# Kernel optimization log

Hardware: AMD Instinct MI355X
Metric: run time of the kernel (lower is better)

The kernel has to match this reference:

```python
import jax, jax.numpy as jnp
import numpy as np

KS = {0: (6, 18), 1: (4, 12)}


def _build_modal_edges(feat, k_set):
    # feat: [N, C] -> H_modal [N, len(k_set)*N]
    N = feat.shape[0]
    f = feat / jnp.linalg.norm(feat, axis=1, keepdims=True).clip(1e-12)
    sim = f @ f.T  # [N, N] cosine similarity
    H_list = []
    cols_base = jnp.arange(N)
    for k in k_set:
        _, knn = jax.lax.top_k(sim, k + 1)  # [N, k+1]
        rows = knn.reshape(-1)
        cols = jnp.repeat(cols_base, k + 1)
        H = jnp.zeros((N, N), dtype=feat.dtype).at[rows, cols].set(1.0)
        H_list.append(H)
    return jnp.concatenate(H_list, axis=1)


def _build_incidence(feat1, feat2):
    # feat1/feat2: [N, C] (batch-mean features) -> H [2N, 5N]
    N = feat1.shape[0]
    H1 = _build_modal_edges(feat1, KS[0])  # [N, 2N]
    H2 = _build_modal_edges(feat2, KS[1])  # [N, 2N]
    E1, E2 = H1.shape[1], H2.shape[1]
    blk = jnp.concatenate([
        jnp.concatenate([H1, jnp.zeros((N, E2), H1.dtype)], axis=1),
        jnp.concatenate([jnp.zeros((N, E1), H2.dtype), H2], axis=1),
    ], axis=0)  # block_diag -> [2N, 4N]
    eye = jnp.eye(N, dtype=H1.dtype)
    H_inter = jnp.concatenate([eye, eye], axis=0)  # [2N, N]
    return jnp.concatenate([blk, H_inter], axis=1)  # [2N, 5N]


def _hgconv(x, H, W):
    # x: [B, 2N, Fin], H: [2N, E], W: [Fout, Fin] (torch Linear, no bias)
    x = jnp.einsum('bnf,of->bno', x, W)
    DV = H.sum(axis=1).clip(1.0)  # [2N]
    DE = H.sum(axis=0).clip(1.0)  # [E]
    H_norm = H / jnp.sqrt(DV)[:, None] / DE[None, :]
    A = H_norm @ H_norm.T  # [2N, 2N]
    x = jnp.einsum('nm,bmo->bno', A, x)
    return jax.nn.relu(x)


def setup_inputs() -> dict:
    key = jax.random.key(0)
    k1, k2, k3, k4 = jax.random.split(key, 4)
    B, N, C, Hd = 4, 2048, 64, 128
    feat_mod1 = jax.random.normal(k1, (B, N, C), dtype=jnp.float32)
    feat_mod2 = jax.random.normal(k2, (B, N, C), dtype=jnp.float32)
    # xavier_uniform bounds for [out, in]
    b1 = float(np.sqrt(6.0 / (Hd + C)))
    b2 = float(np.sqrt(6.0 / (Hd + Hd)))
    W1 = jax.random.uniform(k3, (Hd, C), minval=-b1, maxval=b1, dtype=jnp.float32)
    W2 = jax.random.uniform(k4, (Hd, Hd), minval=-b2, maxval=b2, dtype=jnp.float32)
    return {"feat_mod1": feat_mod1, "feat_mod2": feat_mod2, "W1": W1, "W2": W2}


def reference(feat_mod1, feat_mod2, W1, W2):
    B, N, _ = feat_mod1.shape
    H = jax.lax.stop_gradient(
        _build_incidence(feat_mod1.mean(axis=0), feat_mod2.mean(axis=0)))
    x = jnp.concatenate([feat_mod1, feat_mod2], axis=1)  # [B, 2N, C]
    x = _hgconv(x, H, W1)
    x = _hgconv(x, H, W2)
    return x[:, :N, :], x[:, N:, :]
```

## Files before the change

kernel.cpp:

```cpp
#include <hip/hip_runtime.h>
#include <math.h>

#define NN 2048
#define TWO_N 4096
#define BB 4
#define CC 64
#define HD 128
#define CANDCAP 32
#define NE4 (4 * NN)


__global__ void k_prep(const float* __restrict__ W1, const float* __restrict__ W2,
                       float* __restrict__ W1T, float* __restrict__ W2T) {
    int id = blockIdx.x * 256 + threadIdx.x;
    if (id < HD * CC) {
        int c = id >> 6, k = id & 63;
        W1T[(size_t)k * HD + c] = W1[id];
    }
    {
        int c = id >> 7, k = id & 127;
        W2T[(size_t)k * HD + c] = W2[id];
    }
}

__global__ void k_mean_norm(const float* __restrict__ f1, const float* __restrict__ f2,
                            float* __restrict__ g32T, double* __restrict__ gR64,
                            int* __restrict__ DV) {
    int n = blockIdx.x;
    int m = blockIdx.y;
    int c = threadIdx.x;
    if (m == 0 && n < 64) DV[n * 64 + c] = 0;
    const float* f = m ? f2 : f1;
    double s = 0.0;
    for (int b = 0; b < BB; ++b) s += (double)f[((size_t)(b * NN) + n) * CC + c];
    double mean = s * 0.25;
    double sq = mean * mean;
    for (int d = 32; d >= 1; d >>= 1) sq += __shfl_xor(sq, d);
    double norm = sqrt(sq);
    if (norm < 1e-12) norm = 1e-12;
    double g = mean / norm;
    g32T[((size_t)m * CC + c) * NN + n] = (float)g;
    gR64[((size_t)m * NN + n) * CC + c] = g;
}

__global__ void __launch_bounds__(256)
k_sims(const float* __restrict__ g32T, float* __restrict__ sims) {
    __shared__ float As[CC][64];
    __shared__ float Bs[CC][64];
    __shared__ float Cs[64][65];
    int m  = blockIdx.y;
    int bi = blockIdx.x >> 5, bj = blockIdx.x & 31;
    if (bi > bj) return;
    int i0 = bi * 64, j0 = bj * 64;
    const float* g = g32T + (size_t)m * CC * NN;
    int tid = threadIdx.x;
    #pragma unroll
    for (int q = 0; q < 16; ++q) {
        int idx = q * 256 + tid;
        int k = idx >> 6, r = idx & 63;
        As[k][r] = g[(size_t)k * NN + i0 + r];
        Bs[k][r] = g[(size_t)k * NN + j0 + r];
    }
    __syncthreads();
    int tr = tid >> 4, tc = tid & 15;
    float acc[4][4] = {{0.f}};
    #pragma unroll
    for (int k = 0; k < CC; ++k) {
        float4 a = *((const float4*)&As[k][tr << 2]);
        float4 b = *((const float4*)&Bs[k][tc << 2]);
        acc[0][0] += a.x * b.x; acc[0][1] += a.x * b.y; acc[0][2] += a.x * b.z; acc[0][3] += a.x * b.w;
        acc[1][0] += a.y * b.x; acc[1][1] += a.y * b.y; acc[1][2] += a.y * b.z; acc[1][3] += a.y * b.w;
        acc[2][0] += a.z * b.x; acc[2][1] += a.z * b.y; acc[2][2] += a.z * b.z; acc[2][3] += a.z * b.w;
        acc[3][0] += a.w * b.x; acc[3][1] += a.w * b.y; acc[3][2] += a.w * b.z; acc[3][3] += a.w * b.w;
    }
    float* srow = sims + (size_t)m * NN * NN;
    #pragma unroll
    for (int x = 0; x < 4; ++x) {
        float4 v = make_float4(acc[x][0], acc[x][1], acc[x][2], acc[x][3]);
        *((float4*)&srow[(size_t)(i0 + (tr << 2) + x) * NN + j0 + (tc << 2)]) = v;
        Cs[(tr << 2) + x][(tc << 2) + 0] = acc[x][0];
        Cs[(tr << 2) + x][(tc << 2) + 1] = acc[x][1];
        Cs[(tr << 2) + x][(tc << 2) + 2] = acc[x][2];
        Cs[(tr << 2) + x][(tc << 2) + 3] = acc[x][3];
    }
    __syncthreads();
    #pragma unroll
    for (int q = 0; q < 4; ++q) {
        int idx = q * 256 + tid;
        int cc = idx >> 4, rr4 = (idx & 15) << 2;
        float4 v = make_float4(Cs[rr4 + 0][cc], Cs[rr4 + 1][cc],
                               Cs[rr4 + 2][cc], Cs[rr4 + 3][cc]);
        *((float4*)&srow[(size_t)(j0 + cc) * NN + i0 + rr4]) = v;
    }
}

__global__ void __launch_bounds__(512)
k_selref(const float* __restrict__ sims, const double* __restrict__ gR64,
         int* __restrict__ knn1, int* __restrict__ knn2, int* __restrict__ DV) {
    __shared__ int    candL[8][CANDCAP];
    __shared__ double dotsL[8][CANDCAP];
    int wave = threadIdx.x >> 6, lane = threadIdx.x & 63;
    int row = blockIdx.x * 8 + wave;
    int m = row >> 11, i = row & 2047;
    int K = m ? 13 : 19;
    const float* s = sims + (size_t)m * NN * NN + (size_t)i * NN;
    float sv[32];
    #pragma unroll
    for (int q = 0; q < 8; ++q) {
        float4 v = *((const float4*)&s[q * 256 + (lane << 2)]);
        sv[q * 4 + 0] = v.x; sv[q * 4 + 1] = v.y; sv[q * 4 + 2] = v.z; sv[q * 4 + 3] = v.w;
    }
    float lo = -1.01f, hi = 1.01f;
    for (int it = 0; it < 15; ++it) {
        float t = 0.5f * (lo + hi);
        int cnt = 0;
        #pragma unroll
        for (int r = 0; r < 32; ++r)
            cnt += __popcll(__ballot(sv[r] >= t));
        if (cnt >= K) lo = t; else hi = t;
    }
    float thr = lo - 1e-5f;
    unsigned long long ltmask = (lane == 0) ? 0ull : ((~0ull) >> (64 - lane));
    int base = 0;
    #pragma unroll
    for (int r = 0; r < 32; ++r) {
        int j = ((r >> 2) << 8) + (lane << 2) + (r & 3);
        bool p = sv[r] >= thr;
        unsigned long long mk = __ballot(p);
        int ofs = base + __popcll(mk & ltmask);
        if (p && ofs < CANDCAP) candL[wave][ofs] = j;
        base += __popcll(mk);
    }
    int cnt = (base < CANDCAP) ? base : CANDCAP;
    __syncthreads();
    const double* gm = gR64 + (size_t)m * NN * CC;
    double qc = gm[(size_t)i * CC + lane];
    int t4 = 0;
    for (; t4 + 3 < cnt; t4 += 4) {
        int j0 = candL[wave][t4 + 0], j1 = candL[wave][t4 + 1];
        int j2 = candL[wave][t4 + 2], j3 = candL[wave][t4 + 3];
        double p0 = qc * gm[(size_t)j0 * CC + lane];
        double p1 = qc * gm[(size_t)j1 * CC + lane];
        double p2 = qc * gm[(size_t)j2 * CC + lane];
        double p3 = qc * gm[(size_t)j3 * CC + lane];
        #pragma unroll
        for (int d = 32; d >= 1; d >>= 1) {
            p0 += __shfl_xor(p0, d); p1 += __shfl_xor(p1, d);
            p2 += __shfl_xor(p2, d); p3 += __shfl_xor(p3, d);
        }
        if (lane == 0) {
            dotsL[wave][t4 + 0] = p0; dotsL[wave][t4 + 1] = p1;
            dotsL[wave][t4 + 2] = p2; dotsL[wave][t4 + 3] = p3;
        }
    }
    for (; t4 < cnt; ++t4) {
        int j = candL[wave][t4];
        double p = qc * gm[(size_t)j * CC + lane];
        #pragma unroll
        for (int d = 32; d >= 1; d >>= 1) p += __shfl_xor(p, d);
        if (lane == 0) dotsL[wave][t4] = p;
    }
    __syncthreads();
    int* knn = m ? knn2 : knn1;
    if (lane < cnt) {
        double vt = dotsL[wave][lane]; int jt = candL[wave][lane];
        int rank = 0;
        for (int s2 = 0; s2 < cnt; ++s2) {
            double vs = dotsL[wave][s2]; int js = candL[wave][s2];
            if (vs > vt || (vs == vt && js < jt)) ++rank;
        }
        if (rank < K) {
            knn[(size_t)i * K + rank] = jt;
            int w = (rank < (m ? 5 : 7)) ? 2 : 1;
            atomicAdd(&DV[m ? NN + jt : jt], w);
        }
    }
}

__global__ void k_scan(const int* __restrict__ DV, int* __restrict__ offs,
                       int* __restrict__ cursor, float* __restrict__ dvisf) {
    int lane = threadIdx.x;
    int base = lane * 64;
    int s = 0;
    for (int q = 0; q < 64; ++q) s += DV[base + q];
    int x = s;
    for (int d = 1; d < 64; d <<= 1) {
        int y = __shfl_up(x, d);
        if (lane >= d) x += y;
    }
    int run = x - s;
    for (int q = 0; q < 64; ++q) {
        int v = base + q;
        offs[v] = run; cursor[v] = run;
        dvisf[v] = (float)(1.0 / sqrt((double)(DV[v] + 1)));
        run += DV[v];
    }
    if (lane == 63) offs[TWO_N] = run;
}

__global__ void k_fill(const int* __restrict__ knn1, const int* __restrict__ knn2,
                       int* __restrict__ cursor, int* __restrict__ entries) {
    int id = blockIdx.x * blockDim.x + threadIdx.x;
    const int M1 = NN * 19, M2 = NN * 13;
    if (id < M1) {
        int i = id / 19, t = id % 19;
        int v = knn1[id];
        int p = atomicAdd(&cursor[v], 1); entries[p] = NN + i;
        if (t < 7) { int p2 = atomicAdd(&cursor[v], 1); entries[p2] = i; }
    } else if (id < M1 + M2) {
        int id2 = id - M1;
        int i = id2 / 13, t = id2 % 13;
        int v = NN + knn2[id2];
        int p = atomicAdd(&cursor[v], 1); entries[p] = 3 * NN + i;
        if (t < 5) { int p2 = atomicAdd(&cursor[v], 1); entries[p2] = 2 * NN + i; }
    }
}

__global__ void k_edgeX(const float4* __restrict__ x1, const float4* __restrict__ x2,
                        const float* __restrict__ dvisf,
                        const int* __restrict__ knn1, const int* __restrict__ knn2,
                        float4* __restrict__ u4) {
    __shared__ int mem[19];
    __shared__ float wv[19];
    int blk = blockIdx.x;
    int t = threadIdx.x;
    int f4 = t & 15, b = t >> 4;
    if (blk < NN) {
        if (t < 19) { int v = knn1[(size_t)blk * 19 + t]; mem[t] = v; wv[t] = dvisf[v]; }
        __syncthreads();
        float ax = 0.f, ay = 0.f, az = 0.f, aw = 0.f;
        #pragma unroll
        for (int q = 0; q < 7; ++q) {
            float w = wv[q];
            float4 val = x1[((size_t)(b * NN) + mem[q]) * 16 + f4];
            ax += val.x * w; ay += val.y * w; az += val.z * w; aw += val.w * w;
        }
        const float i7 = 1.f / 49.f;
        u4[(size_t)blk * 64 + t] = make_float4(ax * i7, ay * i7, az * i7, aw * i7);
        #pragma unroll
        for (int q = 7; q < 19; ++q) {
            float w = wv[q];
            float4 val = x1[((size_t)(b * NN) + mem[q]) * 16 + f4];
            ax += val.x * w; ay += val.y * w; az += val.z * w; aw += val.w * w;
        }
        const float i19 = 1.f / 361.f;
        u4[(size_t)(NN + blk) * 64 + t] =
            make_float4(ax * i19, ay * i19, az * i19, aw * i19);
    } else {
        int i = blk - NN;
        if (t < 13) { int j = knn2[(size_t)i * 13 + t]; mem[t] = j; wv[t] = dvisf[NN + j]; }
        __syncthreads();
        float ax = 0.f, ay = 0.f, az = 0.f, aw = 0.f;
        #pragma unroll
        for (int q = 0; q < 5; ++q) {
            float w = wv[q];
            float4 val = x2[((size_t)(b * NN) + mem[q]) * 16 + f4];
            ax += val.x * w; ay += val.y * w; az += val.z * w; aw += val.w * w;
        }
        const float i5 = 1.f / 25.f;
        u4[(size_t)(2 * NN + i) * 64 + t] =
            make_float4(ax * i5, ay * i5, az * i5, aw * i5);
        #pragma unroll
        for (int q = 5; q < 13; ++q) {
            float w = wv[q];
            float4 val = x2[((size_t)(b * NN) + mem[q]) * 16 + f4];
            ax += val.x * w; ay += val.y * w; az += val.z * w; aw += val.w * w;
        }
        const float i13 = 1.f / 169.f;
        u4[(size_t)(3 * NN + i) * 64 + t] =
            make_float4(ax * i13, ay * i13, az * i13, aw * i13);
    }
}

__global__ void k_nodeX(const float4* __restrict__ u4,
                        const float4* __restrict__ x1, const float4* __restrict__ x2,
                        const float* __restrict__ dvisf,
                        const int* __restrict__ offs, const int* __restrict__ entries,
                        float4* __restrict__ aggx4) {
    int v = blockIdx.x;
    int t = threadIdx.x;
    int f4 = t & 15, b = t >> 4;
    int s = offs[v], e_end = offs[v + 1];
    float a0x = 0.f, a0y = 0.f, a0z = 0.f, a0w = 0.f;
    float a1x = 0.f, a1y = 0.f, a1z = 0.f, a1w = 0.f;
    float a2x = 0.f, a2y = 0.f, a2z = 0.f, a2w = 0.f;
    float a3x = 0.f, a3y = 0.f, a3z = 0.f, a3w = 0.f;
    int p = s;
    for (; p + 3 < e_end; p += 4) {
        int e0 = entries[p], e1 = entries[p + 1], e2 = entries[p + 2], e3 = entries[p + 3];
        float4 v0 = u4[(size_t)e0 * 64 + t];
        float4 v1 = u4[(size_t)e1 * 64 + t];
        float4 v2 = u4[(size_t)e2 * 64 + t];
        float4 v3 = u4[(size_t)e3 * 64 + t];
        a0x += v0.x; a0y += v0.y; a0z += v0.z; a0w += v0.w;
        a1x += v1.x; a1y += v1.y; a1z += v1.z; a1w += v1.w;
        a2x += v2.x; a2y += v2.y; a2z += v2.z; a2w += v2.w;
        a3x += v3.x; a3y += v3.y; a3z += v3.z; a3w += v3.w;
    }
    for (; p < e_end; ++p) {
        float4 v0 = u4[(size_t)entries[p] * 64 + t];
        a0x += v0.x; a0y += v0.y; a0z += v0.z; a0w += v0.w;
    }
    float ax = (a0x + a1x) + (a2x + a3x);
    float ay = (a0y + a1y) + (a2y + a3y);
    float az = (a0z + a1z) + (a2z + a3z);
    float aw = (a0w + a1w) + (a2w + a3w);
    int partner = (v < NN) ? v + NN : v - NN;
    float w0 = dvisf[v], w1 = dvisf[partner];
    float4 xv = (v < NN) ? x1[((size_t)(b * NN) + v) * 16 + f4]
                         : x2[((size_t)(b * NN) + (v - NN)) * 16 + f4];
    float4 xp = (partner < NN) ? x1[((size_t)(b * NN) + partner) * 16 + f4]
                               : x2[((size_t)(b * NN) + (partner - NN)) * 16 + f4];
    ax += 0.25f * (xv.x * w0 + xp.x * w1);
    ay += 0.25f * (xv.y * w0 + xp.y * w1);
    az += 0.25f * (xv.z * w0 + xp.z * w1);
    aw += 0.25f * (xv.w * w0 + xp.w * w1);
    ax *= w0; ay *= w0; az *= w0; aw *= w0;
    aggx4[(size_t)v * 64 + t] = make_float4(ax, ay, az, aw);
}

__global__ void __launch_bounds__(256)
k_gemm1R(const float* __restrict__ aggx, const float* __restrict__ W1T,
         float* __restrict__ z) {
    __shared__ float xT[64][33];
    __shared__ float wT[64][132];
    int tid = threadIdx.x;
    int g0 = blockIdx.x * 32;
    #pragma unroll
    for (int q = 0; q < 8; ++q) {
        int idx = q * 256 + tid;
        int row = idx >> 6, k = idx & 63;
        xT[k][row] = aggx[(size_t)(g0 + row) * CC + k];
    }
    #pragma unroll
    for (int q = 0; q < 32; ++q) {
        int idx = q * 256 + tid;
        wT[idx >> 7][idx & 127] = W1T[idx];
    }
    __syncthreads();
    int tr = tid >> 5, tc = tid & 31;
    int r0 = tr * 4, c0 = tc * 4;
    float acc[4][4] = {{0.f}};
    #pragma unroll
    for (int k = 0; k < CC; ++k) {
        float xr0 = xT[k][r0 + 0], xr1 = xT[k][r0 + 1];
        float xr2 = xT[k][r0 + 2], xr3 = xT[k][r0 + 3];
        float4 w = *((const float4*)&wT[k][c0]);
        acc[0][0] += xr0 * w.x; acc[0][1] += xr0 * w.y; acc[0][2] += xr0 * w.z; acc[0][3] += xr0 * w.w;
        acc[1][0] += xr1 * w.x; acc[1][1] += xr1 * w.y; acc[1][2] += xr1 * w.z; acc[1][3] += xr1 * w.w;
        acc[2][0] += xr2 * w.x; acc[2][1] += xr2 * w.y; acc[2][2] += xr2 * w.z; acc[2][3] += xr2 * w.w;
        acc[3][0] += xr3 * w.x; acc[3][1] += xr3 * w.y; acc[3][2] += xr3 * w.z; acc[3][3] += xr3 * w.w;
    }
    #pragma unroll
    for (int i = 0; i < 4; ++i) {
        float4 v = make_float4(fmaxf(acc[i][0], 0.f), fmaxf(acc[i][1], 0.f),
                               fmaxf(acc[i][2], 0.f), fmaxf(acc[i][3], 0.f));
        *((float4*)&z[(size_t)(g0 + r0 + i) * HD + c0]) = v;
    }
}

__global__ void __launch_bounds__(256)
k_gemm2(const float* __restrict__ zin, const float* __restrict__ W2T,
        float* __restrict__ y) {
    __shared__ float zT[64][33];
    __shared__ float wT[64][132];
    int tid = threadIdx.x;
    int g0 = blockIdx.x * 32;
    int tr = tid >> 5, tc = tid & 31;
    int r0 = tr * 4, c0 = tc * 4;
    float acc[4][4] = {{0.f}};
    for (int kc = 0; kc < 2; ++kc) {
        int k0 = kc * 64;
        __syncthreads();
        #pragma unroll
        for (int q = 0; q < 8; ++q) {
            int idx = q * 256 + tid;
            int row = idx >> 6, k = idx & 63;
            zT[k][row] = zin[(size_t)(g0 + row) * HD + k0 + k];
        }
        #pragma unroll
        for (int q = 0; q < 32; ++q) {
            int idx = q * 256 + tid;
            int k = idx >> 7, c = idx & 127;
            wT[k][c] = W2T[(size_t)(k0 + k) * HD + c];
        }
        __syncthreads();
        #pragma unroll
        for (int k = 0; k < 64; ++k) {
            float zr0 = zT[k][r0 + 0], zr1 = zT[k][r0 + 1];
            float zr2 = zT[k][r0 + 2], zr3 = zT[k][r0 + 3];
            float4 w = *((const float4*)&wT[k][c0]);
            acc[0][0] += zr0 * w.x; acc[0][1] += zr0 * w.y; acc[0][2] += zr0 * w.z; acc[0][3] += zr0 * w.w;
            acc[1][0] += zr1 * w.x; acc[1][1] += zr1 * w.y; acc[1][2] += zr1 * w.z; acc[1][3] += zr1 * w.w;
            acc[2][0] += zr2 * w.x; acc[2][1] += zr2 * w.y; acc[2][2] += zr2 * w.z; acc[2][3] += zr2 * w.w;
            acc[3][0] += zr3 * w.x; acc[3][1] += zr3 * w.y; acc[3][2] += zr3 * w.z; acc[3][3] += zr3 * w.w;
        }
    }
    #pragma unroll
    for (int i = 0; i < 4; ++i) {
        float4 v = make_float4(acc[i][0], acc[i][1], acc[i][2], acc[i][3]);
        *((float4*)&y[(size_t)(g0 + r0 + i) * HD + c0]) = v;
    }
}

__global__ void k_edge(const float4* __restrict__ y4, const float* __restrict__ dvisf,
                       const int* __restrict__ knn1, const int* __restrict__ knn2,
                       float4* __restrict__ u4) {
    __shared__ int mem[19];
    __shared__ float wv[19];
    int blk = blockIdx.x;
    int f4 = threadIdx.x & 31;
    int b  = threadIdx.x >> 5;
    int bo = b * 32 + f4;
    int t = threadIdx.x;
    if (blk < NN) {
        if (t < 19) { int v = knn1[(size_t)blk * 19 + t]; mem[t] = v; wv[t] = dvisf[v]; }
        __syncthreads();
        float ax = 0.f, ay = 0.f, az = 0.f, aw = 0.f;
        #pragma unroll
        for (int q = 0; q < 7; ++q) {
            float w = wv[q];
            float4 val = y4[(size_t)mem[q] * 128 + bo];
            ax += val.x * w; ay += val.y * w; az += val.z * w; aw += val.w * w;
        }
        const float i7 = 1.f / 49.f;
        u4[(size_t)blk * 128 + bo] = make_float4(ax * i7, ay * i7, az * i7, aw * i7);
        #pragma unroll
        for (int q = 7; q < 19; ++q) {
            float w = wv[q];
            float4 val = y4[(size_t)mem[q] * 128 + bo];
            ax += val.x * w; ay += val.y * w; az += val.z * w; aw += val.w * w;
        }
        const float i19 = 1.f / 361.f;
        u4[(size_t)(NN + blk) * 128 + bo] =
            make_float4(ax * i19, ay * i19, az * i19, aw * i19);
    } else {
        int i = blk - NN;
        if (t < 13) { int v = NN + knn2[(size_t)i * 13 + t]; mem[t] = v; wv[t] = dvisf[v]; }
        __syncthreads();
        float ax = 0.f, ay = 0.f, az = 0.f, aw = 0.f;
        #pragma unroll
        for (int q = 0; q < 5; ++q) {
            float w = wv[q];
            float4 val = y4[(size_t)mem[q] * 128 + bo];
            ax += val.x * w; ay += val.y * w; az += val.z * w; aw += val.w * w;
        }
        const float i5 = 1.f / 25.f;
        u4[(size_t)(2 * NN + i) * 128 + bo] =
            make_float4(ax * i5, ay * i5, az * i5, aw * i5);
        #pragma unroll
        for (int q = 5; q < 13; ++q) {
            float w = wv[q];
            float4 val = y4[(size_t)mem[q] * 128 + bo];
            ax += val.x * w; ay += val.y * w; az += val.z * w; aw += val.w * w;
        }
        const float i13 = 1.f / 169.f;
        u4[(size_t)(3 * NN + i) * 128 + bo] =
            make_float4(ax * i13, ay * i13, az * i13, aw * i13);
    }
}

__global__ void k_node2(const float4* __restrict__ u4, const float4* __restrict__ y4,
                        const float* __restrict__ dvisf,
                        const int* __restrict__ offs, const int* __restrict__ entries,
                        float4* __restrict__ outp4) {
    int v = blockIdx.x;
    int f4 = threadIdx.x & 31;
    int b  = threadIdx.x >> 5;
    int bo = b * 32 + f4;
    int s = offs[v], e_end = offs[v + 1];
    float a0x = 0.f, a0y = 0.f, a0z = 0.f, a0w = 0.f;
    float a1x = 0.f, a1y = 0.f, a1z = 0.f, a1w = 0.f;
    float a2x = 0.f, a2y = 0.f, a2z = 0.f, a2w = 0.f;
    float a3x = 0.f, a3y = 0.f, a3z = 0.f, a3w = 0.f;
    int p = s;
    for (; p + 3 < e_end; p += 4) {
        int e0 = entries[p], e1 = entries[p + 1], e2 = entries[p + 2], e3 = entries[p + 3];
        float4 v0 = u4[(size_t)e0 * 128 + bo];
        float4 v1 = u4[(size_t)e1 * 128 + bo];
        float4 v2 = u4[(size_t)e2 * 128 + bo];
        float4 v3 = u4[(size_t)e3 * 128 + bo];
        a0x += v0.x; a0y += v0.y; a0z += v0.z; a0w += v0.w;
        a1x += v1.x; a1y += v1.y; a1z += v1.z; a1w += v1.w;
        a2x += v2.x; a2y += v2.y; a2z += v2.z; a2w += v2.w;
        a3x += v3.x; a3y += v3.y; a3z += v3.z; a3w += v3.w;
    }
    for (; p < e_end; ++p) {
        float4 v0 = u4[(size_t)entries[p] * 128 + bo];
        a0x += v0.x; a0y += v0.y; a0z += v0.z; a0w += v0.w;
    }
    float ax = (a0x + a1x) + (a2x + a3x);
    float ay = (a0y + a1y) + (a2y + a3y);
    float az = (a0z + a1z) + (a2z + a3z);
    float aw = (a0w + a1w) + (a2w + a3w);
    int partner = (v < NN) ? v + NN : v - NN;
    float w0 = dvisf[v], w1 = dvisf[partner];
    float4 yv = y4[(size_t)v * 128 + bo];
    float4 yp = y4[(size_t)partner * 128 + bo];
    ax += 0.25f * (yv.x * w0 + yp.x * w1);
    ay += 0.25f * (yv.y * w0 + yp.y * w1);
    az += 0.25f * (yv.z * w0 + yp.z * w1);
    aw += 0.25f * (yv.w * w0 + yp.w * w1);
    ax *= w0; ay *= w0; az *= w0; aw *= w0;
    float4 res = make_float4(fmaxf(ax, 0.f), fmaxf(ay, 0.f),
                             fmaxf(az, 0.f), fmaxf(aw, 0.f));
    size_t o;
    if (v < NN) o = ((size_t)(b * NN + v)) * 32 + f4;
    else        o = (size_t)BB * NN * 32 + ((size_t)(b * NN + (v - NN))) * 32 + f4;
    outp4[o] = res;
}

extern "C" void kernel_launch(void* const* d_in, const int* in_sizes, int n_in,
                              void* d_out, int out_size, void* d_ws, size_t ws_size,
                              hipStream_t stream) {
    const float* f1 = (const float*)d_in[0];
    const float* f2 = (const float*)d_in[1];
    const float* W1 = (const float*)d_in[2];
    const float* W2 = (const float*)d_in[3];
    float* out = (float*)d_out;

    char* ws = (char*)d_ws;
    size_t off = 0;
    auto alloc = [&](size_t bytes) -> void* {
        void* p = ws + off;
        off = (off + bytes + 255) & ~(size_t)255;
        return p;
    };
    float*  g32T    = (float*)alloc((size_t)2 * CC * NN * 4);
    double* gR64    = (double*)alloc((size_t)2 * NN * CC * 8);
    float*  sims    = (float*)alloc((size_t)2 * NN * NN * 4);
    float*  ybuf    = (float*)alloc((size_t)BB * TWO_N * HD * 4);
    float*  zbuf    = (float*)alloc((size_t)BB * TWO_N * HD * 4);
    float*  ubuf    = (float*)alloc((size_t)BB * NE4 * HD * 4);
    float*  aggx    = (float*)alloc((size_t)BB * TWO_N * CC * 4);
    float*  W1T     = (float*)alloc((size_t)CC * HD * 4);
    float*  W2T     = (float*)alloc((size_t)HD * HD * 4);
    float*  dvisf   = (float*)alloc((size_t)TWO_N * 4);
    int*    knn1    = (int*)alloc((size_t)NN * 19 * 4);
    int*    knn2    = (int*)alloc((size_t)NN * 13 * 4);
    int*    DV      = (int*)alloc((size_t)TWO_N * 4);
    int*    offs    = (int*)alloc((size_t)(TWO_N + 1) * 4);
    int*    cursor  = (int*)alloc((size_t)TWO_N * 4);
    int*    entries = (int*)alloc((size_t)(NN * 26 + NN * 18) * 4);

    k_prep<<<64, 256, 0, stream>>>(W1, W2, W1T, W2T);
    k_mean_norm<<<dim3(NN, 2), 64, 0, stream>>>(f1, f2, g32T, gR64, DV);
    k_sims<<<dim3(32 * 32, 2), 256, 0, stream>>>(g32T, sims);
    k_selref<<<TWO_N / 8, 512, 0, stream>>>(sims, gR64, knn1, knn2, DV);
    k_scan<<<1, 64, 0, stream>>>(DV, offs, cursor, dvisf);
    k_fill<<<(NN * 19 + NN * 13 + 255) / 256, 256, 0, stream>>>(knn1, knn2, cursor, entries);

    k_edgeX<<<2 * NN, 64, 0, stream>>>((const float4*)f1, (const float4*)f2, dvisf,
                                       knn1, knn2, (float4*)ubuf);
    k_nodeX<<<TWO_N, 64, 0, stream>>>((const float4*)ubuf, (const float4*)f1,
                                      (const float4*)f2, dvisf, offs, entries,
                                      (float4*)aggx);
    k_gemm1R<<<(BB * TWO_N) / 32, 256, 0, stream>>>(aggx, W1T, zbuf);

    k_gemm2<<<(BB * TWO_N) / 32, 256, 0, stream>>>(zbuf, W2T, ybuf);
    k_edge<<<2 * NN, 128, 0, stream>>>((const float4*)ybuf, dvisf, knn1, knn2, (float4*)ubuf);
    k_node2<<<TWO_N, 128, 0, stream>>>((const float4*)ubuf, (const float4*)ybuf, dvisf,
                                       offs, entries, (float4*)out);
}
```

Before: 212.6 us.

## Store similarities in bf16, intermediates in fp16, and fuse node aggregation with both GEMMs

Similarity matrices are now stored as bf16 instead of fp32, halving their write and read traffic, and the bisection threshold search uses fewer iterations with a wider candidate margin. Input features, edge aggregates and hidden activations are kept in fp16 buffers. The weight transpose is folded into the mean/norm kernel. Node aggregation, the first GEMM with ReLU and the second GEMM are fused into one kernel, removing two global round trips and two launches. The cost is reduced precision in intermediates, and the wider margin may let in more candidates and overflow the fixed candidate cap.

```diff
diff --git a/kernel.cpp b/kernel.cpp
--- a/kernel.cpp
+++ b/kernel.cpp
@@ -7,32 +7,45 @@
 #define CC 64
 #define HD 128
 #define CANDCAP 32
-#define NE4 (4 * NN)
-
-
-__global__ void k_prep(const float* __restrict__ W1, const float* __restrict__ W2,
-                       float* __restrict__ W1T, float* __restrict__ W2T) {
-    int id = blockIdx.x * 256 + threadIdx.x;
-    if (id < HD * CC) {
-        int c = id >> 6, k = id & 63;
-        W1T[(size_t)k * HD + c] = W1[id];
-    }
-    {
-        int c = id >> 7, k = id & 127;
-        W2T[(size_t)k * HD + c] = W2[id];
-    }
+
+typedef unsigned short u16;
+typedef _Float16 h16;
+union H4 { ushort4 u; h16 h[4]; };
+
+__device__ __forceinline__ u16 f2bf(float x) {
+    unsigned u = __float_as_uint(x);
+    u += 0x7FFFu + ((u >> 16) & 1u);
+    return (u16)(u >> 16);
 }
 
 __global__ void k_mean_norm(const float* __restrict__ f1, const float* __restrict__ f2,
+                            const float* __restrict__ W1, const float* __restrict__ W2,
                             float* __restrict__ g32T, double* __restrict__ gR64,
+                            u16* __restrict__ xh,
+                            float* __restrict__ W1T, float* __restrict__ W2T,
                             int* __restrict__ DV) {
     int n = blockIdx.x;
     int m = blockIdx.y;
     int c = threadIdx.x;
     if (m == 0 && n < 64) DV[n * 64 + c] = 0;
+    if (m == 1) {
+        if (n < 128) {
+            int idx = n * 64 + c;
+            W1T[(size_t)(idx & 63) * HD + (idx >> 6)] = W1[idx];
+        } else if (n < 384) {
+            int idx = (n - 128) * 64 + c;
+            W2T[(size_t)(idx & 127) * HD + (idx >> 7)] = W2[idx];
+        }
+    }
     const float* f = m ? f2 : f1;
+    float xv[BB];
     double s = 0.0;
-    for (int b = 0; b < BB; ++b) s += (double)f[((size_t)(b * NN) + n) * CC + c];
+    for (int b = 0; b < BB; ++b) {
+        float v = f[((size_t)(b * NN) + n) * CC + c];
+        xv[b] = v; s += (double)v;
+    }
+    h16* xrow = (h16*)(xh + ((size_t)(m * NN + n)) * (BB * CC));
+    for (int b = 0; b < BB; ++b) xrow[b * CC + c] = (h16)xv[b];
     double mean = s * 0.25;
     double sq = mean * mean;
     for (int d = 32; d >= 1; d >>= 1) sq += __shfl_xor(sq, d);
@@ -44,10 +57,9 @@
 }
 
 __global__ void __launch_bounds__(256)
-k_sims(const float* __restrict__ g32T, float* __restrict__ sims) {
-    __shared__ float As[CC][64];
-    __shared__ float Bs[CC][64];
-    __shared__ float Cs[64][65];
+k_sims(const float* __restrict__ g32T, u16* __restrict__ simsbf) {
+    __shared__ float As[64 * 64];
+    __shared__ float Bs[64 * 64];
     int m  = blockIdx.y;
     int bi = blockIdx.x >> 5, bj = blockIdx.x & 31;
     if (bi > bj) return;
@@ -58,44 +70,49 @@
     for (int q = 0; q < 16; ++q) {
         int idx = q * 256 + tid;
         int k = idx >> 6, r = idx & 63;
-        As[k][r] = g[(size_t)k * NN + i0 + r];
-        Bs[k][r] = g[(size_t)k * NN + j0 + r];
+        As[k * 64 + r] = g[(size_t)k * NN + i0 + r];
+        Bs[k * 64 + r] = g[(size_t)k * NN + j0 + r];
     }
     __syncthreads();
     int tr = tid >> 4, tc = tid & 15;
     float acc[4][4] = {{0.f}};
     #pragma unroll
     for (int k = 0; k < CC; ++k) {
-        float4 a = *((const float4*)&As[k][tr << 2]);
-        float4 b = *((const float4*)&Bs[k][tc << 2]);
+        float4 a = *((const float4*)&As[k * 64 + (tr << 2)]);
+        float4 b = *((const float4*)&Bs[k * 64 + (tc << 2)]);
         acc[0][0] += a.x * b.x; acc[0][1] += a.x * b.y; acc[0][2] += a.x * b.z; acc[0][3] += a.x * b.w;
         acc[1][0] += a.y * b.x; acc[1][1] += a.y * b.y; acc[1][2] += a.y * b.z; acc[1][3] += a.y * b.w;
         acc[2][0] += a.z * b.x; acc[2][1] += a.z * b.y; acc[2][2] += a.z * b.z; acc[2][3] += a.z * b.w;
         acc[3][0] += a.w * b.x; acc[3][1] += a.w * b.y; acc[3][2] += a.w * b.z; acc[3][3] += a.w * b.w;
     }
-    float* srow = sims + (size_t)m * NN * NN;
+    __syncthreads();
+    u16* Cs = (u16*)As;
+    u16* srow = simsbf + (size_t)m * NN * NN;
     #pragma unroll
     for (int x = 0; x < 4; ++x) {
-        float4 v = make_float4(acc[x][0], acc[x][1], acc[x][2], acc[x][3]);
-        *((float4*)&srow[(size_t)(i0 + (tr << 2) + x) * NN + j0 + (tc << 2)]) = v;
-        Cs[(tr << 2) + x][(tc << 2) + 0] = acc[x][0];
-        Cs[(tr << 2) + x][(tc << 2) + 1] = acc[x][1];
-        Cs[(tr << 2) + x][(tc << 2) + 2] = acc[x][2];
-        Cs[(tr << 2) + x][(tc << 2) + 3] = acc[x][3];
+        ushort4 vd;
+        vd.x = f2bf(acc[x][0]); vd.y = f2bf(acc[x][1]);
+        vd.z = f2bf(acc[x][2]); vd.w = f2bf(acc[x][3]);
+        *((ushort4*)&srow[(size_t)(i0 + (tr << 2) + x) * NN + j0 + (tc << 2)]) = vd;
+        int cr = ((tr << 2) + x) * 66 + (tc << 2);
+        Cs[cr + 0] = vd.x; Cs[cr + 1] = vd.y; Cs[cr + 2] = vd.z; Cs[cr + 3] = vd.w;
     }
     __syncthreads();
     #pragma unroll
     for (int q = 0; q < 4; ++q) {
         int idx = q * 256 + tid;
         int cc = idx >> 4, rr4 = (idx & 15) << 2;
-        float4 v = make_float4(Cs[rr4 + 0][cc], Cs[rr4 + 1][cc],
-                               Cs[rr4 + 2][cc], Cs[rr4 + 3][cc]);
-        *((float4*)&srow[(size_t)(j0 + cc) * NN + i0 + rr4]) = v;
+        ushort4 vd;
+        vd.x = Cs[(rr4 + 0) * 66 + cc];
+        vd.y = Cs[(rr4 + 1) * 66 + cc];
+        vd.z = Cs[(rr4 + 2) * 66 + cc];
+        vd.w = Cs[(rr4 + 3) * 66 + cc];
+        *((ushort4*)&srow[(size_t)(j0 + cc) * NN + i0 + rr4]) = vd;
     }
 }
 
 __global__ void __launch_bounds__(512)
-k_selref(const float* __restrict__ sims, const double* __restrict__ gR64,
+k_selref(const u16* __restrict__ simsbf, const double* __restrict__ gR64,
          int* __restrict__ knn1, int* __restrict__ knn2, int* __restrict__ DV) {
     __shared__ int    candL[8][CANDCAP];
     __shared__ double dotsL[8][CANDCAP];
@@ -103,28 +120,35 @@
     int row = blockIdx.x * 8 + wave;
     int m = row >> 11, i = row & 2047;
     int K = m ? 13 : 19;
-    const float* s = sims + (size_t)m * NN * NN + (size_t)i * NN;
+    const u16* s = simsbf + (size_t)m * NN * NN + (size_t)i * NN;
     float sv[32];
     #pragma unroll
-    for (int q = 0; q < 8; ++q) {
-        float4 v = *((const float4*)&s[q * 256 + (lane << 2)]);
-        sv[q * 4 + 0] = v.x; sv[q * 4 + 1] = v.y; sv[q * 4 + 2] = v.z; sv[q * 4 + 3] = v.w;
+    for (int q = 0; q < 4; ++q) {
+        uint4 w = *((const uint4*)(s + q * 512 + (lane << 3)));
+        sv[q*8+0] = __uint_as_float(w.x << 16);
+        sv[q*8+1] = __uint_as_float(w.x & 0xFFFF0000u);
+        sv[q*8+2] = __uint_as_float(w.y << 16);
+        sv[q*8+3] = __uint_as_float(w.y & 0xFFFF0000u);
+        sv[q*8+4] = __uint_as_float(w.z << 16);
+        sv[q*8+5] = __uint_as_float(w.z & 0xFFFF0000u);
+        sv[q*8+6] = __uint_as_float(w.w << 16);
+        sv[q*8+7] = __uint_as_float(w.w & 0xFFFF0000u);
     }
     float lo = -1.01f, hi = 1.01f;
-    for (int it = 0; it < 15; ++it) {
+    for (int it = 0; it < 12; ++it) {
         float t = 0.5f * (lo + hi);
-        int cnt = 0;
+        int c = 0;
         #pragma unroll
         for (int r = 0; r < 32; ++r)
-            cnt += __popcll(__ballot(sv[r] >= t));
-        if (cnt >= K) lo = t; else hi = t;
-    }
-    float thr = lo - 1e-5f;
+            c += __popcll(__ballot(sv[r] >= t));
+        if (c >= K) lo = t; else hi = t;
+    }
+    float thr = lo - 6e-3f;
     unsigned long long ltmask = (lane == 0) ? 0ull : ((~0ull) >> (64 - lane));
     int base = 0;
     #pragma unroll
     for (int r = 0; r < 32; ++r) {
-        int j = ((r >> 2) << 8) + (lane << 2) + (r & 3);
+        int j = ((r >> 3) << 9) + (lane << 3) + (r & 7);
         bool p = sv[r] >= thr;
         unsigned long long mk = __ballot(p);
         int ofs = base + __popcll(mk & ltmask);
@@ -137,12 +161,12 @@
     double qc = gm[(size_t)i * CC + lane];
     int t4 = 0;
     for (; t4 + 3 < cnt; t4 += 4) {
-        int j0 = candL[wave][t4 + 0], j1 = candL[wave][t4 + 1];
-        int j2 = candL[wave][t4 + 2], j3 = candL[wave][t4 + 3];
-        double p0 = qc * gm[(size_t)j0 * CC + lane];
-        double p1 = qc * gm[(size_t)j1 * CC + lane];
-        double p2 = qc * gm[(size_t)j2 * CC + lane];
-        double p3 = qc * gm[(size_t)j3 * CC + lane];
+        int j0c = candL[wave][t4 + 0], j1c = candL[wave][t4 + 1];
+        int j2c = candL[wave][t4 + 2], j3c = candL[wave][t4 + 3];
+        double p0 = qc * gm[(size_t)j0c * CC + lane];
+        double p1 = qc * gm[(size_t)j1c * CC + lane];
+        double p2 = qc * gm[(size_t)j2c * CC + lane];
+        double p3 = qc * gm[(size_t)j3c * CC + lane];
         #pragma unroll
         for (int d = 32; d >= 1; d >>= 1) {
             p0 += __shfl_xor(p0, d); p1 += __shfl_xor(p1, d);
@@ -216,298 +240,287 @@
     }
 }
 
-__global__ void k_edgeX(const float4* __restrict__ x1, const float4* __restrict__ x2,
-                        const float* __restrict__ dvisf,
+__global__ void k_edgeX(const u16* __restrict__ xh, const float* __restrict__ dvisf,
                         const int* __restrict__ knn1, const int* __restrict__ knn2,
-                        float4* __restrict__ u4) {
+                        u16* __restrict__ uh1) {
+    int blk = blockIdx.x;
+    int t = threadIdx.x;
+    int off = t * 4;
+    if (blk < NN) {
+        int mv = 0; float wv = 0.f;
+        if (t < 19) { mv = knn1[(size_t)blk * 19 + t]; wv = dvisf[mv]; }
+        float a0=0,a1=0,a2=0,a3=0;
+        #pragma unroll
+        for (int q = 0; q < 7; ++q) {
+            int mq = __shfl(mv, q); float wq = __shfl(wv, q);
+            H4 hv; hv.u = *((const ushort4*)(xh + (size_t)mq * 256 + off));
+            a0 += (float)hv.h[0]*wq; a1 += (float)hv.h[1]*wq;
+            a2 += (float)hv.h[2]*wq; a3 += (float)hv.h[3]*wq;
+        }
+        { H4 ho; ho.h[0]=(h16)(a0*(1.f/49.f)); ho.h[1]=(h16)(a1*(1.f/49.f));
+          ho.h[2]=(h16)(a2*(1.f/49.f)); ho.h[3]=(h16)(a3*(1.f/49.f));
+          *((ushort4*)(uh1 + (size_t)blk * 256 + off)) = ho.u; }
+        #pragma unroll
+        for (int q = 7; q < 19; ++q) {
+            int mq = __shfl(mv, q); float wq = __shfl(wv, q);
+            H4 hv; hv.u = *((const ushort4*)(xh + (size_t)mq * 256 + off));
+            a0 += (float)hv.h[0]*wq; a1 += (float)hv.h[1]*wq;
+            a2 += (float)hv.h[2]*wq; a3 += (float)hv.h[3]*wq;
+        }
+        { H4 ho; ho.h[0]=(h16)(a0*(1.f/361.f)); ho.h[1]=(h16)(a1*(1.f/361.f));
+          ho.h[2]=(h16)(a2*(1.f/361.f)); ho.h[3]=(h16)(a3*(1.f/361.f));
+          *((ushort4*)(uh1 + (size_t)(NN + blk) * 256 + off)) = ho.u; }
+    } else {
+        int i = blk - NN;
+        int mv = 0; float wv = 0.f;
+        if (t < 13) { mv = knn2[(size_t)i * 13 + t]; wv = dvisf[NN + mv]; }
+        float a0=0,a1=0,a2=0,a3=0;
+        #pragma unroll
+        for (int q = 0; q < 5; ++q) {
+            int mq = __shfl(mv, q); float wq = __shfl(wv, q);
+            H4 hv; hv.u = *((const ushort4*)(xh + (size_t)(NN + mq) * 256 + off));
+            a0 += (float)hv.h[0]*wq; a1 += (float)hv.h[1]*wq;
+            a2 += (float)hv.h[2]*wq; a3 += (float)hv.h[3]*wq;
+        }
+        { H4 ho; ho.h[0]=(h16)(a0*(1.f/25.f)); ho.h[1]=(h16)(a1*(1.f/25.f));
+          ho.h[2]=(h16)(a2*(1.f/25.f)); ho.h[3]=(h16)(a3*(1.f/25.f));
+          *((ushort4*)(uh1 + (size_t)(2 * NN + i) * 256 + off)) = ho.u; }
+        #pragma unroll
+        for (int q = 5; q < 13; ++q) {
+            int mq = __shfl(mv, q); float wq = __shfl(wv, q);
+            H4 hv; hv.u = *((const ushort4*)(xh + (size_t)(NN + mq) * 256 + off));
+            a0 += (float)hv.h[0]*wq; a1 += (float)hv.h[1]*wq;
+            a2 += (float)hv.h[2]*wq; a3 += (float)hv.h[3]*wq;
+        }
+        { H4 ho; ho.h[0]=(h16)(a0*(1.f/169.f)); ho.h[1]=(h16)(a1*(1.f/169.f));
+          ho.h[2]=(h16)(a2*(1.f/169.f)); ho.h[3]=(h16)(a3*(1.f/169.f));
+          *((ushort4*)(uh1 + (size_t)(3 * NN + i) * 256 + off)) = ho.u; }
+    }
+}
+
+__global__ void __launch_bounds__(256)
+k_nodeGemm(const u16* __restrict__ uh1,
+           const float* __restrict__ f1, const float* __restrict__ f2,
+           const float* __restrict__ dvisf,
+           const int* __restrict__ offs, const int* __restrict__ entries,
+           const float* __restrict__ W1T, const float* __restrict__ W2T,
+           u16* __restrict__ yh) {
+    __shared__ float wT[64 * 132];
+    __shared__ float xT[64 * 33];
+    __shared__ float zT[128 * 33];
+    int tid = threadIdx.x;
+    int bid = blockIdx.x;
+    int v0 = bid * 8, g0 = bid * 32;
+    #pragma unroll
+    for (int p = 0; p < 32; ++p) {
+        int idx = p * 256 + tid;
+        wT[(idx >> 7) * 132 + (idx & 127)] = W1T[idx];
+    }
+    const float4* x1 = (const float4*)f1;
+    const float4* x2 = (const float4*)f2;
+    #pragma unroll
+    for (int it = 0; it < 2; ++it) {
+        int item = it * 256 + tid;
+        int vl = item >> 6, l6 = item & 63;
+        int b = l6 >> 4, f4i = l6 & 15;
+        int c4 = f4i << 2;
+        int v = v0 + vl;
+        int s = offs[v], e_end = offs[v + 1];
+        float A0[4] = {0,0,0,0}, A1[4] = {0,0,0,0};
+        float A2[4] = {0,0,0,0}, A3[4] = {0,0,0,0};
+        int p = s;
+        for (; p + 3 < e_end; p += 4) {
+            H4 h0, h1, h2, h3;
+            h0.u = *((const ushort4*)(uh1 + (size_t)entries[p+0] * 256 + l6 * 4));
+            h1.u = *((const ushort4*)(uh1 + (size_t)entries[p+1] * 256 + l6 * 4));
+            h2.u = *((const ushort4*)(uh1 + (size_t)entries[p+2] * 256 + l6 * 4));
+            h3.u = *((const ushort4*)(uh1 + (size_t)entries[p+3] * 256 + l6 * 4));
+            #pragma unroll
+            for (int j = 0; j < 4; ++j) {
+                A0[j] += (float)h0.h[j]; A1[j] += (float)h1.h[j];
+                A2[j] += (float)h2.h[j]; A3[j] += (float)h3.h[j];
+            }
+        }
+        for (; p < e_end; ++p) {
+            H4 h0; h0.u = *((const ushort4*)(uh1 + (size_t)entries[p] * 256 + l6 * 4));
+            #pragma unroll
+            for (int j = 0; j < 4; ++j) A0[j] += (float)h0.h[j];
+        }
+        float r[4];
+        #pragma unroll
+        for (int j = 0; j < 4; ++j) r[j] = (A0[j] + A1[j]) + (A2[j] + A3[j]);
+        int partner = (v < NN) ? v + NN : v - NN;
+        float w0 = dvisf[v], w1 = dvisf[partner];
+        float4 xv = (v < NN) ? x1[((size_t)(b * NN) + v) * 16 + f4i]
+                             : x2[((size_t)(b * NN) + (v - NN)) * 16 + f4i];
+        float4 xp = (partner < NN) ? x1[((size_t)(b * NN) + partner) * 16 + f4i]
+                                   : x2[((size_t)(b * NN) + (partner - NN)) * 16 + f4i];
+        r[0] += 0.25f * (xv.x * w0 + xp.x * w1);
+        r[1] += 0.25f * (xv.y * w0 + xp.y * w1);
+        r[2] += 0.25f * (xv.z * w0 + xp.z * w1);
+        r[3] += 0.25f * (xv.w * w0 + xp.w * w1);
+        int rloc = vl * 4 + b;
+        #pragma unroll
+        for (int j = 0; j < 4; ++j) xT[(c4 + j) * 33 + rloc] = r[j] * w0;
+    }
+    __syncthreads();
+    int tr = tid >> 5, tc = tid & 31;
+    int r0 = tr * 4, c0 = tc * 4;
+    {
+        float acc[4][4] = {{0.f}};
+        #pragma unroll
+        for (int k = 0; k < CC; ++k) {
+            float xr0 = xT[k*33 + r0+0], xr1 = xT[k*33 + r0+1];
+            float xr2 = xT[k*33 + r0+2], xr3 = xT[k*33 + r0+3];
+            float4 w = *((const float4*)&wT[k * 132 + c0]);
+            acc[0][0]+=xr0*w.x; acc[0][1]+=xr0*w.y; acc[0][2]+=xr0*w.z; acc[0][3]+=xr0*w.w;
+            acc[1][0]+=xr1*w.x; acc[1][1]+=xr1*w.y; acc[1][2]+=xr1*w.z; acc[1][3]+=xr1*w.w;
+            acc[2][0]+=xr2*w.x; acc[2][1]+=xr2*w.y; acc[2][2]+=xr2*w.z; acc[2][3]+=xr2*w.w;
+            acc[3][0]+=xr3*w.x; acc[3][1]+=xr3*w.y; acc[3][2]+=xr3*w.z; acc[3][3]+=xr3*w.w;
+        }
+        #pragma unroll
+        for (int i = 0; i < 4; ++i)
+            #pragma unroll
+            for (int j = 0; j < 4; ++j)
+                zT[(c0 + j) * 33 + r0 + i] = fmaxf(acc[i][j], 0.f);
+    }
+    float acc2[4][4] = {{0.f}};
+    for (int kc = 0; kc < 2; ++kc) {
+        __syncthreads();
+        #pragma unroll
+        for (int p = 0; p < 32; ++p) {
+            int idx = p * 256 + tid;
+            int k = idx >> 7, c = idx & 127;
+            wT[k * 132 + c] = W2T[(size_t)(kc * 64 + k) * HD + c];
+        }
+        __syncthreads();
+        #pragma unroll
+        for (int k = 0; k < 64; ++k) {
+            int kk = kc * 64 + k;
+            float zr0 = zT[kk*33 + r0+0], zr1 = zT[kk*33 + r0+1];
+            float zr2 = zT[kk*33 + r0+2], zr3 = zT[kk*33 + r0+3];
+            float4 w = *((const float4*)&wT[k * 132 + c0]);
+            acc2[0][0]+=zr0*w.x; acc2[0][1]+=zr0*w.y; acc2[0][2]+=zr0*w.z; acc2[0][3]+=zr0*w.w;
+            acc2[1][0]+=zr1*w.x; acc2[1][1]+=zr1*w.y; acc2[1][2]+=zr1*w.z; acc2[1][3]+=zr1*w.w;
+            acc2[2][0]+=zr2*w.x; acc2[2][1]+=zr2*w.y; acc2[2][2]+=zr2*w.z; acc2[2][3]+=zr2*w.w;
+            acc2[3][0]+=zr3*w.x; acc2[3][1]+=zr3*w.y; acc2[3][2]+=zr3*w.z; acc2[3][3]+=zr3*w.w;
+        }
+    }
+    #pragma unroll
+    for (int i = 0; i < 4; ++i) {
+        H4 ho;
+        ho.h[0] = (h16)acc2[i][0]; ho.h[1] = (h16)acc2[i][1];
+        ho.h[2] = (h16)acc2[i][2]; ho.h[3] = (h16)acc2[i][3];
+        *((ushort4*)(yh + (size_t)(g0 + r0 + i) * HD + c0)) = ho.u;
+    }
+}
+
+__global__ void k_edge2(const u16* __restrict__ yh, const float* __restrict__ dvisf,
+                        const int* __restrict__ knn1, const int* __restrict__ knn2,
+                        u16* __restrict__ uh2) {
     __shared__ int mem[19];
     __shared__ float wv[19];
     int blk = blockIdx.x;
     int t = threadIdx.x;
-    int f4 = t & 15, b = t >> 4;
+    int off = t * 4;
     if (blk < NN) {
         if (t < 19) { int v = knn1[(size_t)blk * 19 + t]; mem[t] = v; wv[t] = dvisf[v]; }
         __syncthreads();
-        float ax = 0.f, ay = 0.f, az = 0.f, aw = 0.f;
+        float a0=0,a1=0,a2=0,a3=0;
         #pragma unroll
         for (int q = 0; q < 7; ++q) {
             float w = wv[q];
-            float4 val = x1[((size_t)(b * NN) + mem[q]) * 16 + f4];
-            ax += val.x * w; ay += val.y * w; az += val.z * w; aw += val.w * w;
-        }
-        const float i7 = 1.f / 49.f;
-        u4[(size_t)blk * 64 + t] = make_float4(ax * i7, ay * i7, az * i7, aw * i7);
+            H4 hv; hv.u = *((const ushort4*)(yh + (size_t)mem[q] * 512 + off));
+            a0 += (float)hv.h[0]*w; a1 += (float)hv.h[1]*w;
+            a2 += (float)hv.h[2]*w; a3 += (float)hv.h[3]*w;
+        }
+        { H4 ho; ho.h[0]=(h16)(a0*(1.f/49.f)); ho.h[1]=(h16)(a1*(1.f/49.f));
+          ho.h[2]=(h16)(a2*(1.f/49.f)); ho.h[3]=(h16)(a3*(1.f/49.f));
+          *((ushort4*)(uh2 + (size_t)blk * 512 + off)) = ho.u; }
         #pragma unroll
         for (int q = 7; q < 19; ++q) {
             float w = wv[q];
-            float4 val = x1[((size_t)(b * NN) + mem[q]) * 16 + f4];
-            ax += val.x * w; ay += val.y * w; az += val.z * w; aw += val.w * w;
-        }
-        const float i19 = 1.f / 361.f;
-        u4[(size_t)(NN + blk) * 64 + t] =
-            make_float4(ax * i19, ay * i19, az * i19, aw * i19);
-    } else {
-        int i = blk - NN;
-        if (t < 13) { int j = knn2[(size_t)i * 13 + t]; mem[t] = j; wv[t] = dvisf[NN + j]; }
-        __syncthreads();
-        float ax = 0.f, ay = 0.f, az = 0.f, aw = 0.f;
-        #pragma unroll
-        for (int q = 0; q < 5; ++q) {
-            float w = wv[q];
-            float4 val = x2[((size_t)(b * NN) + mem[q]) * 16 + f4];
-            ax += val.x * w; ay += val.y * w; az += val.z * w; aw += val.w * w;
-        }
-        const float i5 = 1.f / 25.f;
-        u4[(size_t)(2 * NN + i) * 64 + t] =
-            make_float4(ax * i5, ay * i5, az * i5, aw * i5);
-        #pragma unroll
-        for (int q = 5; q < 13; ++q) {
-            float w = wv[q];
-            float4 val = x2[((size_t)(b * NN) + mem[q]) * 16 + f4];
-            ax += val.x * w; ay += val.y * w; az += val.z * w; aw += val.w * w;
-        }
-        const float i13 = 1.f / 169.f;
-        u4[(size_t)(3 * NN + i) * 64 + t] =
-            make_float4(ax * i13, ay * i13, az * i13, aw * i13);
-    }
-}
-
-__global__ void k_nodeX(const float4* __restrict__ u4,
-                        const float4* __restrict__ x1, const float4* __restrict__ x2,
-                        const float* __restrict__ dvisf,
-                        const int* __restrict__ offs, const int* __restrict__ entries,
-                        float4* __restrict__ aggx4) {
-    int v = blockIdx.x;
-    int t = threadIdx.x;
-    int f4 = t & 15, b = t >> 4;
-    int s = offs[v], e_end = offs[v + 1];
-    float a0x = 0.f, a0y = 0.f, a0z = 0.f, a0w = 0.f;
-    float a1x = 0.f, a1y = 0.f, a1z = 0.f, a1w = 0.f;
-    float a2x = 0.f, a2y = 0.f, a2z = 0.f, a2w = 0.f;
-    float a3x = 0.f, a3y = 0.f, a3z = 0.f, a3w = 0.f;
-    int p = s;
-    for (; p + 3 < e_end; p += 4) {
-        int e0 = entries[p], e1 = entries[p + 1], e2 = entries[p + 2], e3 = entries[p + 3];
-        float4 v0 = u4[(size_t)e0 * 64 + t];
-        float4 v1 = u4[(size_t)e1 * 64 + t];
-        float4 v2 = u4[(size_t)e2 * 64 + t];
-        float4 v3 = u4[(size_t)e3 * 64 + t];
-        a0x += v0.x; a0y += v0.y; a0z += v0.z; a0w += v0.w;
-        a1x += v1.x; a1y += v1.y; a1z += v1.z; a1w += v1.w;
-        a2x += v2.x; a2y += v2.y; a2z += v2.z; a2w += v2.w;
-        a3x += v3.x; a3y += v3.y; a3z += v3.z; a3w += v3.w;
-    }
-    for (; p < e_end; ++p) {
-        float4 v0 = u4[(size_t)entries[p] * 64 + t];
-        a0x += v0.x; a0y += v0.y; a0z += v0.z; a0w += v0.w;
-    }
-    float ax = (a0x + a1x) + (a2x + a3x);
-    float ay = (a0y + a1y) + (a2y + a3y);
-    float az = (a0z + a1z) + (a2z + a3z);
-    float aw = (a0w + a1w) + (a2w + a3w);
-    int partner = (v < NN) ? v + NN : v - NN;
-    float w0 = dvisf[v], w1 = dvisf[partner];
-    float4 xv = (v < NN) ? x1[((size_t)(b * NN) + v) * 16 + f4]
-                         : x2[((size_t)(b * NN) + (v - NN)) * 16 + f4];
-    float4 xp = (partner < NN) ? x1[((size_t)(b * NN) + partner) * 16 + f4]
-                               : x2[((size_t)(b * NN) + (partner - NN)) * 16 + f4];
-    ax += 0.25f * (xv.x * w0 + xp.x * w1);
-    ay += 0.25f * (xv.y * w0 + xp.y * w1);
-    az += 0.25f * (xv.z * w0 + xp.z * w1);
-    aw += 0.25f * (xv.w * w0 + xp.w * w1);
-    ax *= w0; ay *= w0; az *= w0; aw *= w0;
-    aggx4[(size_t)v * 64 + t] = make_float4(ax, ay, az, aw);
-}
-
-__global__ void __launch_bounds__(256)
-k_gemm1R(const float* __restrict__ aggx, const float* __restrict__ W1T,
-         float* __restrict__ z) {
-    __shared__ float xT[64][33];
-    __shared__ float wT[64][132];
-    int tid = threadIdx.x;
-    int g0 = blockIdx.x * 32;
-    #pragma unroll
-    for (int q = 0; q < 8; ++q) {
-        int idx = q * 256 + tid;
-        int row = idx >> 6, k = idx & 63;
-        xT[k][row] = aggx[(size_t)(g0 + row) * CC + k];
-    }
-    #pragma unroll
-    for (int q = 0; q < 32; ++q) {
-        int idx = q * 256 + tid;
-        wT[idx >> 7][idx & 127] = W1T[idx];
-    }
-    __syncthreads();
-    int tr = tid >> 5, tc = tid & 31;
-    int r0 = tr * 4, c0 = tc * 4;
-    float acc[4][4] = {{0.f}};
-    #pragma unroll
-    for (int k = 0; k < CC; ++k) {
-        float xr0 = xT[k][r0 + 0], xr1 = xT[k][r0 + 1];
-        float xr2 = xT[k][r0 + 2], xr3 = xT[k][r0 + 3];
-        float4 w = *((const float4*)&wT[k][c0]);
-        acc[0][0] += xr0 * w.x; acc[0][1] += xr0 * w.y; acc[0][2] += xr0 * w.z; acc[0][3] += xr0 * w.w;
-        acc[1][0] += xr1 * w.x; acc[1][1] += xr1 * w.y; acc[1][2] += xr1 * w.z; acc[1][3] += xr1 * w.w;
-        acc[2][0] += xr2 * w.x; acc[2][1] += xr2 * w.y; acc[2][2] += xr2 * w.z; acc[2][3] += xr2 * w.w;
-        acc[3][0] += xr3 * w.x; acc[3][1] += xr3 * w.y; acc[3][2] += xr3 * w.z; acc[3][3] += xr3 * w.w;
-    }
-    #pragma unroll
-    for (int i = 0; i < 4; ++i) {
-        float4 v = make_float4(fmaxf(acc[i][0], 0.f), fmaxf(acc[i][1], 0.f),
-                               fmaxf(acc[i][2], 0.f), fmaxf(acc[i][3], 0.f));
-        *((float4*)&z[(size_t)(g0 + r0 + i) * HD + c0]) = v;
-    }
-}
-
-__global__ void __launch_bounds__(256)
-k_gemm2(const float* __restrict__ zin, const float* __restrict__ W2T,
-        float* __restrict__ y) {
-    __shared__ float zT[64][33];
-    __shared__ float wT[64][132];
-    int tid = threadIdx.x;
-    int g0 = blockIdx.x * 32;
-    int tr = tid >> 5, tc = tid & 31;
-    int r0 = tr * 4, c0 = tc * 4;
-    float acc[4][4] = {{0.f}};
-    for (int kc = 0; kc < 2; ++kc) {
-        int k0 = kc * 64;
-        __syncthreads();
-        #pragma unroll
-        for (int q = 0; q < 8; ++q) {
-            int idx = q * 256 + tid;
-            int row = idx >> 6, k = idx & 63;
-            zT[k][row] = zin[(size_t)(g0 + row) * HD + k0 + k];
-        }
-        #pragma unroll
-        for (int q = 0; q < 32; ++q) {
-            int idx = q * 256 + tid;
-            int k = idx >> 7, c = idx & 127;
-            wT[k][c] = W2T[(size_t)(k0 + k) * HD + c];
-        }
-        __syncthreads();
-        #pragma unroll
-        for (int k = 0; k < 64; ++k) {
-            float zr0 = zT[k][r0 + 0], zr1 = zT[k][r0 + 1];
-            float zr2 = zT[k][r0 + 2], zr3 = zT[k][r0 + 3];
-            float4 w = *((const float4*)&wT[k][c0]);
-            acc[0][0] += zr0 * w.x; acc[0][1] += zr0 * w.y; acc[0][2] += zr0 * w.z; acc[0][3] += zr0 * w.w;
-            acc[1][0] += zr1 * w.x; acc[1][1] += zr1 * w.y; acc[1][2] += zr1 * w.z; acc[1][3] += zr1 * w.w;
-            acc[2][0] += zr2 * w.x; acc[2][1] += zr2 * w.y; acc[2][2] += zr2 * w.z; acc[2][3] += zr2 * w.w;
-            acc[3][0] += zr3 * w.x; acc[3][1] += zr3 * w.y; acc[3][2] += zr3 * w.z; acc[3][3] += zr3 * w.w;
-        }
-    }
-    #pragma unroll
-    for (int i = 0; i < 4; ++i) {
-        float4 v = make_float4(acc[i][0], acc[i][1], acc[i][2], acc[i][3]);
-        *((float4*)&y[(size_t)(g0 + r0 + i) * HD + c0]) = v;
-    }
-}
-
-__global__ void k_edge(const float4* __restrict__ y4, const float* __restrict__ dvisf,
-                       const int* __restrict__ knn1, const int* __restrict__ knn2,
-                       float4* __restrict__ u4) {
-    __shared__ int mem[19];
-    __shared__ float wv[19];
-    int blk = blockIdx.x;
-    int f4 = threadIdx.x & 31;
-    int b  = threadIdx.x >> 5;
-    int bo = b * 32 + f4;
-    int t = threadIdx.x;
-    if (blk < NN) {
-        if (t < 19) { int v = knn1[(size_t)blk * 19 + t]; mem[t] = v; wv[t] = dvisf[v]; }
-        __syncthreads();
-        float ax = 0.f, ay = 0.f, az = 0.f, aw = 0.f;
-        #pragma unroll
-        for (int q = 0; q < 7; ++q) {
-            float w = wv[q];
-            float4 val = y4[(size_t)mem[q] * 128 + bo];
-            ax += val.x * w; ay += val.y * w; az += val.z * w; aw += val.w * w;
-        }
-        const float i7 = 1.f / 49.f;
-        u4[(size_t)blk * 128 + bo] = make_float4(ax * i7, ay * i7, az * i7, aw * i7);
-        #pragma unroll
-        for (int q = 7; q < 19; ++q) {
-            float w = wv[q];
-            float4 val = y4[(size_t)mem[q] * 128 + bo];
-            ax += val.x * w; ay += val.y * w; az += val.z * w; aw += val.w * w;
-        }
-        const float i19 = 1.f / 361.f;
-        u4[(size_t)(NN + blk) * 128 + bo] =
-            make_float4(ax * i19, ay * i19, az * i19, aw * i19);
+            H4 hv; hv.u = *((const ushort4*)(yh + (size_t)mem[q] * 512 + off));
+            a0 += (float)hv.h[0]*w; a1 += (float)hv.h[1]*w;
+            a2 += (float)hv.h[2]*w; a3 += (float)hv.h[3]*w;
+        }
+        { H4 ho; ho.h[0]=(h16)(a0*(1.f/361.f)); ho.h[1]=(h16)(a1*(1.f/361.f));
+          ho.h[2]=(h16)(a2*(1.f/361.f)); ho.h[3]=(h16)(a3*(1.f/361.f));
+          *((ushort4*)(uh2 + (size_t)(NN + blk) * 512 + off)) = ho.u; }
     } else {
         int i = blk - NN;
         if (t < 13) { int v = NN + knn2[(size_t)i * 13 + t]; mem[t] = v; wv[t] = dvisf[v]; }
         __syncthreads();
-        float ax = 0.f, ay = 0.f, az = 0.f, aw = 0.f;
+        float a0=0,a1=0,a2=0,a3=0;
         #pragma unroll
         for (int q = 0; q < 5; ++q) {
             float w = wv[q];
-            float4 val = y4[(size_t)mem[q] * 128 + bo];
-            ax += val.x * w; ay += val.y * w; az += val.z * w; aw += val.w * w;
-        }
-        const float i5 = 1.f / 25.f;
-        u4[(size_t)(2 * NN + i) * 128 + bo] =
-            make_float4(ax * i5, ay * i5, az * i5, aw * i5);
+            H4 hv; hv.u = *((const ushort4*)(yh + (size_t)mem[q] * 512 + off));
+            a0 += (float)hv.h[0]*w; a1 += (float)hv.h[1]*w;
+            a2 += (float)hv.h[2]*w; a3 += (float)hv.h[3]*w;
+        }
+        { H4 ho; ho.h[0]=(h16)(a0*(1.f/25.f)); ho.h[1]=(h16)(a1*(1.f/25.f));
+          ho.h[2]=(h16)(a2*(1.f/25.f)); ho.h[3]=(h16)(a3*(1.f/25.f));
+          *((ushort4*)(uh2 + (size_t)(2 * NN + i) * 512 + off)) = ho.u; }
         #pragma unroll
         for (int q = 5; q < 13; ++q) {
             float w = wv[q];
-            float4 val = y4[(size_t)mem[q] * 128 + bo];
-            ax += val.x * w; ay += val.y * w; az += val.z * w; aw += val.w * w;
-        }
-        const float i13 = 1.f / 169.f;
-        u4[(size_t)(3 * NN + i) * 128 + bo] =
-            make_float4(ax * i13, ay * i13, az * i13, aw * i13);
-    }
-}
-
-__global__ void k_node2(const float4* __restrict__ u4, const float4* __restrict__ y4,
+            H4 hv; hv.u = *((const ushort4*)(yh + (size_t)mem[q] * 512 + off));
+            a0 += (float)hv.h[0]*w; a1 += (float)hv.h[1]*w;
+            a2 += (float)hv.h[2]*w; a3 += (float)hv.h[3]*w;
+        }
+        { H4 ho; ho.h[0]=(h16)(a0*(1.f/169.f)); ho.h[1]=(h16)(a1*(1.f/169.f));
+          ho.h[2]=(h16)(a2*(1.f/169.f)); ho.h[3]=(h16)(a3*(1.f/169.f));
+          *((ushort4*)(uh2 + (size_t)(3 * NN + i) * 512 + off)) = ho.u; }
+    }
+}
+
+__global__ void k_node2(const u16* __restrict__ uh2, const u16* __restrict__ yh,
                         const float* __restrict__ dvisf,
                         const int* __restrict__ offs, const int* __restrict__ entries,
-                        float4* __restrict__ outp4) {
+                        float* __restrict__ out) {
     int v = blockIdx.x;
-    int f4 = threadIdx.x & 31;
-    int b  = threadIdx.x >> 5;
-    int bo = b * 32 + f4;
+    int t = threadIdx.x;
+    int off = t * 4;
     int s = offs[v], e_end = offs[v + 1];
-    float a0x = 0.f, a0y = 0.f, a0z = 0.f, a0w = 0.f;
-    float a1x = 0.f, a1y = 0.f, a1z = 0.f, a1w = 0.f;
-    float a2x = 0.f, a2y = 0.f, a2z = 0.f, a2w = 0.f;
-    float a3x = 0.f, a3y = 0.f, a3z = 0.f, a3w = 0.f;
+    float A0[4] = {0,0,0,0}, A1[4] = {0,0,0,0};
+    float A2[4] = {0,0,0,0}, A3[4] = {0,0,0,0};
     int p = s;
     for (; p + 3 < e_end; p += 4) {
-        int e0 = entries[p], e1 = entries[p + 1], e2 = entries[p + 2], e3 = entries[p + 3];
-        float4 v0 = u4[(size_t)e0 * 128 + bo];
-        float4 v1 = u4[(size_t)e1 * 128 + bo];
-        float4 v2 = u4[(size_t)e2 * 128 + bo];
-        float4 v3 = u4[(size_t)e3 * 128 + bo];
-        a0x += v0.x; a0y += v0.y; a0z += v0.z; a0w += v0.w;
-        a1x += v1.x; a1y += v1.y; a1z += v1.z; a1w += v1.w;
-        a2x += v2.x; a2y += v2.y; a2z += v2.z; a2w += v2.w;
-        a3x += v3.x; a3y += v3.y; a3z += v3.z; a3w += v3.w;
+        H4 h0, h1, h2, h3;
+        h0.u = *((const ushort4*)(uh2 + (size_t)entries[p+0] * 512 + off));
+        h1.u = *((const ushort4*)(uh2 + (size_t)entries[p+1] * 512 + off));
+        h2.u = *((const ushort4*)(uh2 + (size_t)entries[p+2] * 512 + off));
+        h3.u = *((const ushort4*)(uh2 + (size_t)entries[p+3] * 512 + off));
+        #pragma unroll
+        for (int j = 0; j < 4; ++j) {
+            A0[j] += (float)h0.h[j]; A1[j] += (float)h1.h[j];
+            A2[j] += (float)h2.h[j]; A3[j] += (float)h3.h[j];
+        }
     }
     for (; p < e_end; ++p) {
-        float4 v0 = u4[(size_t)entries[p] * 128 + bo];
-        a0x += v0.x; a0y += v0.y; a0z += v0.z; a0w += v0.w;
-    }
-    float ax = (a0x + a1x) + (a2x + a3x);
-    float ay = (a0y + a1y) + (a2y + a3y);
-    float az = (a0z + a1z) + (a2z + a3z);
-    float aw = (a0w + a1w) + (a2w + a3w);
+        H4 h0; h0.u = *((const ushort4*)(uh2 + (size_t)entries[p] * 512 + off));
+        #pragma unroll
+        for (int j = 0; j < 4; ++j) A0[j] += (float)h0.h[j];
+    }
+    float r[4];
+    #pragma unroll
+    for (int j = 0; j < 4; ++j) r[j] = (A0[j] + A1[j]) + (A2[j] + A3[j]);
     int partner = (v < NN) ? v + NN : v - NN;
     float w0 = dvisf[v], w1 = dvisf[partner];
-    float4 yv = y4[(size_t)v * 128 + bo];
-    float4 yp = y4[(size_t)partner * 128 + bo];
-    ax += 0.25f * (yv.x * w0 + yp.x * w1);
-    ay += 0.25f * (yv.y * w0 + yp.y * w1);
-    az += 0.25f * (yv.z * w0 + yp.z * w1);
-    aw += 0.25f * (yv.w * w0 + yp.w * w1);
-    ax *= w0; ay *= w0; az *= w0; aw *= w0;
-    float4 res = make_float4(fmaxf(ax, 0.f), fmaxf(ay, 0.f),
-                             fmaxf(az, 0.f), fmaxf(aw, 0.f));
-    size_t o;
-    if (v < NN) o = ((size_t)(b * NN + v)) * 32 + f4;
-    else        o = (size_t)BB * NN * 32 + ((size_t)(b * NN + (v - NN))) * 32 + f4;
-    outp4[o] = res;
+    H4 yv, yp;
+    yv.u = *((const ushort4*)(yh + (size_t)v * 512 + off));
+    yp.u = *((const ushort4*)(yh + (size_t)partner * 512 + off));
+    #pragma unroll
+    for (int j = 0; j < 4; ++j) {
+        r[j] += 0.25f * ((float)yv.h[j] * w0 + (float)yp.h[j] * w1);
+        r[j] = fmaxf(r[j] * w0, 0.f);
+    }
+    int b = t >> 5, f4i = t & 31;
+    size_t o4;
+    if (v < NN) o4 = ((size_t)(b * NN + v)) * 32 + f4i;
+    else        o4 = (size_t)BB * NN * 32 + ((size_t)(b * NN + (v - NN))) * 32 + f4i;
+    ((float4*)out)[o4] = make_float4(r[0], r[1], r[2], r[3]);
 }
 
 extern "C" void kernel_launch(void* const* d_in, const int* in_sizes, int n_in,
@@ -526,39 +539,34 @@
         off = (off + bytes + 255) & ~(size_t)255;
         return p;
     };
-    float*  g32T    = (float*)alloc((size_t)2 * CC * NN * 4);
-    double* gR64    = (double*)alloc((size_t)2 * NN * CC * 8);
-    float*  sims    = (float*)alloc((size_t)2 * NN * NN * 4);
-    float*  ybuf    = (float*)alloc((size_t)BB * TWO_N * HD * 4);
-    float*  zbuf    = (float*)alloc((size_t)BB * TWO_N * HD * 4);
-    float*  ubuf    = (float*)alloc((size_t)BB * NE4 * HD * 4);
-    float*  aggx    = (float*)alloc((size_t)BB * TWO_N * CC * 4);
-    float*  W1T     = (float*)alloc((size_t)CC * HD * 4);
-    float*  W2T     = (float*)alloc((size_t)HD * HD * 4);
-    float*  dvisf   = (float*)alloc((size_t)TWO_N * 4);
-    int*    knn1    = (int*)alloc((size_t)NN * 19 * 4);
-    int*    knn2    = (int*)alloc((size_t)NN * 13 * 4);
-    int*    DV      = (int*)alloc((size_t)TWO_N * 4);
-    int*    offs    = (int*)alloc((size_t)(TWO_N + 1) * 4);
-    int*    cursor  = (int*)alloc((size_t)TWO_N * 4);
-    int*    entries = (int*)alloc((size_t)(NN * 26 + NN * 18) * 4);
-
-    k_prep<<<64, 256, 0, stream>>>(W1, W2, W1T, W2T);
-    k_mean_norm<<<dim3(NN, 2), 64, 0, stream>>>(f1, f2, g32T, gR64, DV);
-    k_sims<<<dim3(32 * 32, 2), 256, 0, stream>>>(g32T, sims);
-    k_selref<<<TWO_N / 8, 512, 0, stream>>>(sims, gR64, knn1, knn2, DV);
+    float*  g32T   = (float*)alloc((size_t)2 * CC * NN * 4);
+    double* gR64   = (double*)alloc((size_t)2 * NN * CC * 8);
+    u16*    simsbf = (u16*)alloc((size_t)2 * NN * NN * 2);
+    u16*    xh     = (u16*)alloc((size_t)TWO_N * BB * CC * 2);
+    u16*    uh1    = (u16*)alloc((size_t)4 * NN * BB * CC * 2);
+    u16*    yh     = (u16*)alloc((size_t)TWO_N * BB * HD * 2);
+    u16*    uh2    = (u16*)alloc((size_t)4 * NN * BB * HD * 2);
+    float*  W1T    = (float*)alloc((size_t)CC * HD * 4);
+    float*  W2T    = (float*)alloc((size_t)HD * HD * 4);
+    float*  dvisf  = (float*)alloc((size_t)TWO_N * 4);
+    int*    knn1   = (int*)alloc((size_t)NN * 19 * 4);
+    int*    knn2   = (int*)alloc((size_t)NN * 13 * 4);
+    int*    DV     = (int*)alloc((size_t)TWO_N * 4);
+    int*    offs   = (int*)alloc((size_t)(TWO_N + 1) * 4);
+    int*    cursor = (int*)alloc((size_t)TWO_N * 4);
+    int*    entries= (int*)alloc((size_t)(NN * 26 + NN * 18) * 4);
+
+    k_mean_norm<<<dim3(NN, 2), 64, 0, stream>>>(f1, f2, W1, W2, g32T, gR64,
+                                                xh, W1T, W2T, DV);
+    k_sims<<<dim3(32 * 32, 2), 256, 0, stream>>>(g32T, simsbf);
+    k_selref<<<TWO_N / 8, 512, 0, stream>>>(simsbf, gR64, knn1, knn2, DV);
     k_scan<<<1, 64, 0, stream>>>(DV, offs, cursor, dvisf);
     k_fill<<<(NN * 19 + NN * 13 + 255) / 256, 256, 0, stream>>>(knn1, knn2, cursor, entries);
 
-    k_edgeX<<<2 * NN, 64, 0, stream>>>((const float4*)f1, (const float4*)f2, dvisf,
-                                       knn1, knn2, (float4*)ubuf);
-    k_nodeX<<<TWO_N, 64, 0, stream>>>((const float4*)ubuf, (const float4*)f1,
-                                      (const float4*)f2, dvisf, offs, entries,
-                                      (float4*)aggx);
-    k_gemm1R<<<(BB * TWO_N) / 32, 256, 0, stream>>>(aggx, W1T, zbuf);
-
-    k_gemm2<<<(BB * TWO_N) / 32, 256, 0, stream>>>(zbuf, W2T, ybuf);
-    k_edge<<<2 * NN, 128, 0, stream>>>((const float4*)ybuf, dvisf, knn1, knn2, (float4*)ubuf);
-    k_node2<<<TWO_N, 128, 0, stream>>>((const float4*)ubuf, (const float4*)ybuf, dvisf,
-                                       offs, entries, (float4*)out);
-}
+    k_edgeX<<<2 * NN, 64, 0, stream>>>(xh, dvisf, knn1, knn2, uh1);
+    k_nodeGemm<<<(BB * TWO_N) / 32, 256, 0, stream>>>(uh1, f1, f2, dvisf, offs,
+                                                      entries, W1T, W2T, yh);
+
+    k_edge2<<<2 * NN, 128, 0, stream>>>(yh, dvisf, knn1, knn2, uh2);
+    k_node2<<<TWO_N, 128, 0, stream>>>(uh2, yh, dvisf, offs, entries, out);
+}
```

Result: faster. 200.1 us (-5.9%).
